# Optimization experiments

Hardware: AMD Instinct MI355X
Metric: run time of the kernel (lower is better)

Reference implementation:

```python
import jax, jax.numpy as jnp
import numpy as np

B, L, S, D, H, E, UV = 4, 2048, 2048, 1024, 8, 128, 128
ROT_DIM = H * E  # RotaryEmbedding(dim=qk_size*n_heads) applied on flattened dim


def gelu(x):
    return jax.nn.gelu(x, approximate=False)  # torch nn.GELU default (erf)


def rope(x):
    # x: [B, T, ROT_DIM]; interleaved-pair rotary (lucidrains rotary_embedding_torch default)
    T = x.shape[1]
    inv_freq = 1.0 / (10000.0 ** (jnp.arange(0, ROT_DIM, 2, dtype=jnp.float32) / ROT_DIM))
    freqs = jnp.arange(T, dtype=jnp.float32)[:, None] * inv_freq  # [T, ROT_DIM/2]
    cos = jnp.repeat(jnp.cos(freqs), 2, axis=-1)  # [T, ROT_DIM]
    sin = jnp.repeat(jnp.sin(freqs), 2, axis=-1)
    xp = x.reshape(*x.shape[:-1], ROT_DIM // 2, 2)
    x_rot = jnp.stack([-xp[..., 1], xp[..., 0]], axis=-1).reshape(x.shape)
    return x * cos + x_rot * sin


def setup_inputs() -> dict:
    key = jax.random.key(0)
    ks = jax.random.split(key, 16)
    n = lambda k, sh, s=1.0: jax.random.normal(k, sh, jnp.float32) * s
    w = 0.02
    return {
        "u": n(ks[0], (B, L, D)),
        "queries": n(ks[1], (B, L, D)),
        "keys": n(ks[2], (B, S, D)),
        "values": n(ks[3], (B, S, D)),
        "Wqk": n(ks[4], (D, H * E), w), "bqk": jnp.zeros((H * E,), jnp.float32),
        "Wv": n(ks[5], (D, H * UV), w), "bv": jnp.zeros((H * UV,), jnp.float32),
        "Wu": n(ks[6], (D, H * UV), w), "bu": jnp.zeros((H * UV,), jnp.float32),
        "Wo": n(ks[7], (H * UV, D), w), "bo": jnp.zeros((D,), jnp.float32),
        "q_gamma": jnp.ones((E,), jnp.float32), "q_beta": n(ks[8], (E,), w),
        "k_gamma": jnp.ones((E,), jnp.float32), "k_beta": n(ks[9], (E,), w),
    }


def _forward(u, queries, keys, values, Wqk, bqk, Wv, bv, Wu, bu, Wo, bo,
             q_gamma, q_beta, k_gamma, k_beta):
    # use_aff=True: shared qk projection + per-branch ScaleOffset over qk_size
    qk = gelu(queries @ Wqk + bqk)                      # [B,L,H*E]
    qk4 = qk.reshape(B, L, H, E)
    q = (qk4 * q_gamma + q_beta).reshape(B, L, H * E)
    k = (qk4 * k_gamma + k_beta).reshape(B, L, H * E)
    q = rope(q).reshape(B, L, H, E)
    k = rope(k).reshape(B, S, H, E)
    v = gelu(values @ Wv + bv).reshape(B, S, H, UV)
    # Conv1d(kernel_size=1) == pointwise linear over channels
    u_p = gelu(u @ Wu + bu).reshape(B, L, H, UV)
    scale = 1.0 / jnp.sqrt(jnp.float32(E))
    scores = jnp.einsum("blhe,bshe->bhls", q, k) * scale
    attn = jax.nn.softmax(scores, axis=-1)              # [B,H,L,S]
    ctx = jnp.einsum("bhls,bshd->blhd", attn, v)        # [B,L,H,UV]
    out = (u_p * ctx).reshape(B, L, H * UV)             # gate by u
    o = out @ Wo + bo                                   # [B,L,D]
    return o, attn


def reference(u, queries, keys, values, Wqk, bqk, Wv, bv, Wu, bu, Wo, bo,
              q_gamma, q_beta, k_gamma, k_beta):
    return _forward(u, queries, keys, values, Wqk, bqk, Wv, bv, Wu, bu, Wo, bo,
                    q_gamma, q_beta, k_gamma, k_beta)
```

## Files before the change

### kernel.cpp

```cpp
#include <hip/hip_runtime.h>
#include <hip/hip_bf16.h>
#include <math.h>

#define DEVI static __device__ __forceinline__

typedef __attribute__((ext_vector_type(4))) float f32x4;
typedef __attribute__((ext_vector_type(16))) float f32x16;
typedef __attribute__((ext_vector_type(8))) short bf16x8;
typedef __attribute__((ext_vector_type(4))) short bf16x4;

constexpr int Bc = 4, Lc = 2048, Sc = 2048, Dc = 1024, Hc = 8, Ec = 128, UVc = 128;
constexpr int HEc = Hc * Ec;
constexpr int BLc = Bc * Lc;

#define QSC (1.44269504088896340f / 11.31370849898476039f)

DEVI unsigned f2bf_bits(float f) {
  unsigned u = __builtin_bit_cast(unsigned, f);
  return (u + 0x7FFFu + ((u >> 16) & 1u)) >> 16;
}
DEVI short f2bf(float f) { return (short)f2bf_bits(f); }
DEVI float bf2f(short s) {
  return __builtin_bit_cast(float, (unsigned)((unsigned short)s) << 16);
}
DEVI float gelu_f(float x) { return 0.5f * x * (1.0f + erff(x * 0.7071067811865476f)); }

DEVI void gload16(const void* gsrc, void* ldst) {
  __builtin_amdgcn_global_load_lds(
      (const __attribute__((address_space(1))) unsigned*)gsrc,
      (__attribute__((address_space(3))) unsigned*)(ldst), 16, 0, 0);
}

DEVI f32x4 mfma16(bf16x8 a, bf16x8 b, f32x4 c) {
  return __builtin_amdgcn_mfma_f32_16x16x32_bf16(a, b, c, 0, 0, 0);
}
DEVI f32x16 mfma32(bf16x8 a, bf16x8 b, f32x16 c) {
  return __builtin_amdgcn_mfma_f32_32x32x16_bf16(a, b, c, 0, 0, 0);
}

__global__ void cvt3_kernel(const float* __restrict__ i0, const float* __restrict__ i1,
                            const float* __restrict__ i2, short* __restrict__ o0,
                            short* __restrict__ o1, short* __restrict__ o2) {
  const float* ins[3] = {i0, i1, i2};
  short* outs[3] = {o0, o1, o2};
  const float* in = ins[blockIdx.y];
  short* out = outs[blockIdx.y];
  size_t i = ((size_t)blockIdx.x * 256 + threadIdx.x) * 8;
  float4 f1 = *reinterpret_cast<const float4*>(in + i);
  float4 f2 = *reinterpret_cast<const float4*>(in + i + 4);
  uint4 pk;
  pk.x = f2bf_bits(f1.x) | (f2bf_bits(f1.y) << 16);
  pk.y = f2bf_bits(f1.z) | (f2bf_bits(f1.w) << 16);
  pk.z = f2bf_bits(f2.x) | (f2bf_bits(f2.y) << 16);
  pk.w = f2bf_bits(f2.z) | (f2bf_bits(f2.w) << 16);
  *reinterpret_cast<uint4*>(out + i) = pk;
}

__global__ void wt_trans_kernel(const float* __restrict__ W0, const float* __restrict__ W1,
                                const float* __restrict__ W2, const float* __restrict__ W3,
                                short* __restrict__ T0, short* __restrict__ T1,
                                short* __restrict__ T2, short* __restrict__ T3) {
  __shared__ float t[32][33];
  const float* Ws[4] = {W0, W1, W2, W3};
  short* Ts[4] = {T0, T1, T2, T3};
  const float* W = Ws[blockIdx.z];
  short* WT = Ts[blockIdx.z];
  int tx = threadIdx.x, ty = threadIdx.y;
  int n0 = blockIdx.x * 32, k0 = blockIdx.y * 32;
#pragma unroll
  for (int i = 0; i < 4; i++) {
    int r = ty + i * 8;
    t[r][tx] = W[(size_t)(k0 + r) * 1024 + n0 + tx];
  }
  __syncthreads();
#pragma unroll
  for (int i = 0; i < 4; i++) {
    int r = ty + i * 8;
    WT[(size_t)(n0 + r) * 1024 + k0 + tx] = f2bf(t[tx][r]);
  }
}

__global__ void rope_cs_kernel(float2* __restrict__ cs) {
  int idx = blockIdx.x * 256 + threadIdx.x;
  int t = idx >> 9, i = idx & 511;
  float inv = expf((float)i * (-9.210340371976184f / 512.0f));
  float sv, cv;
  sincosf((float)t * inv, &sv, &cv);
  cs[idx] = make_float2(cv, sv);
}

template <int EPI>
__global__ __launch_bounds__(256, 3) void gemm_kernel(
    const short* __restrict__ A, const short* __restrict__ BT,
    const float* __restrict__ bias, void* __restrict__ Cptr, int M, int N, int K) {
  __shared__ char smem[49152];
  const int tid = threadIdx.x;
  const int wave = tid >> 6, lane = tid & 63;
  const int lquad = lane >> 4, l15 = lane & 15;
  const int m0 = blockIdx.x * 128, n0 = blockIdx.y * 128;
  const int wr = wave >> 1, wc = wave & 1;
  f32x4 acc[4][4] = {};

  const int q0 = tid * 16, q1 = tid * 16 + 4096;
  const int r0 = q0 >> 6, o0 = (q0 & 63) ^ ((r0 & 3) << 4);
  const int r1 = q1 >> 6, o1 = (q1 & 63) ^ ((r1 & 3) << 4);
  const short* a0 = A + (size_t)(m0 + r0) * K + (o0 >> 1);
  const short* a1 = A + (size_t)(m0 + r1) * K + (o1 >> 1);
  const short* b0 = BT + (size_t)(n0 + r0) * K + (o0 >> 1);
  const short* b1 = BT + (size_t)(n0 + r1) * K + (o1 >> 1);

#define G_STAGE(buf, kt)                     \
  {                                          \
    char* As_ = smem + (buf)*8192;           \
    char* Bs_ = smem + 24576 + (buf)*8192;   \
    gload16(a0 + (kt), As_ + q0);            \
    gload16(a1 + (kt), As_ + q1);            \
    gload16(b0 + (kt), Bs_ + q0);            \
    gload16(b1 + (kt), Bs_ + q1);            \
  }

  G_STAGE(0, 0);
  G_STAGE(1, 32);
  asm volatile("s_waitcnt vmcnt(4)" ::: "memory");
  __builtin_amdgcn_s_barrier();

  const int NT = K >> 5;
  int cur = 0;
  for (int t = 0; t < NT; t++) {
    int nb = cur + 2;
    if (nb >= 3) nb -= 3;
    G_STAGE(nb, (t + 2 < NT) ? (t + 2) * 32 : 0);
    __builtin_amdgcn_sched_barrier(0);
    const char* As_ = smem + cur * 8192;
    const char* Bs_ = smem + 24576 + cur * 8192;
    const int ko = lquad * 16;
    bf16x8 a[4], b[4];
#pragma unroll
    for (int f = 0; f < 4; f++) {
      int ra = wr * 64 + f * 16 + l15;
      a[f] = *reinterpret_cast<const bf16x8*>(As_ + ra * 64 + (ko ^ ((ra & 3) << 4)));
      int rb = wc * 64 + f * 16 + l15;
      b[f] = *reinterpret_cast<const bf16x8*>(Bs_ + rb * 64 + (ko ^ ((rb & 3) << 4)));
    }
#pragma unroll
    for (int mf = 0; mf < 4; mf++)
#pragma unroll
      for (int nf = 0; nf < 4; nf++)
        acc[mf][nf] = mfma16(a[mf], b[nf], acc[mf][nf]);
    asm volatile("s_waitcnt vmcnt(4) lgkmcnt(0)" ::: "memory");
    __builtin_amdgcn_sched_barrier(0);
    __builtin_amdgcn_s_barrier();
    cur = (cur == 2) ? 0 : cur + 1;
  }
#undef G_STAGE

#pragma unroll
  for (int mf = 0; mf < 4; mf++) {
#pragma unroll
    for (int nf = 0; nf < 4; nf++) {
      const int mrow = m0 + wr * 64 + mf * 16 + 4 * lquad;
      const int ncol = n0 + wc * 64 + nf * 16 + l15;
      const float bval = bias[ncol];
      if constexpr (EPI == 3) {
        int hh = ncol >> 7, dd = ncol & 127;
        int bb = mrow >> 11, ss = mrow & 2047;
        bf16x4 gv;
#pragma unroll
        for (int r = 0; r < 4; r++) gv[r] = f2bf(gelu_f(acc[mf][nf][r] + bval));
        *reinterpret_cast<bf16x4*>((short*)Cptr + (((size_t)bb * 8 + hh) * 128 + dd) * 2048 + ss) = gv;
      } else if constexpr (EPI == 1) {
#pragma unroll
        for (int r = 0; r < 4; r++)
          ((short*)Cptr)[(size_t)(mrow + r) * N + ncol] = f2bf(gelu_f(acc[mf][nf][r] + bval));
      } else {
#pragma unroll
        for (int r = 0; r < 4; r++)
          ((float*)Cptr)[(size_t)(mrow + r) * N + ncol] = acc[mf][nf][r] + bval;
      }
    }
  }
}

__global__ void rope_apply_kernel(const short* __restrict__ qkg,
                                  const float2* __restrict__ cstab,
                                  const float* __restrict__ qg, const float* __restrict__ qb,
                                  const float* __restrict__ kg, const float* __restrict__ kb,
                                  short* __restrict__ qo, short* __restrict__ ko) {
  int tid = blockIdx.x * 256 + threadIdx.x;
  size_t base = (size_t)tid * 8;
  int bl = (int)(base >> 10);
  int rem = (int)(base & 1023);
  int e0 = rem & 127;
  int t = bl & 2047;
  int pf = rem >> 1;
  uint4 raw = *reinterpret_cast<const uint4*>(qkg + base);
  short sh[8];
  *reinterpret_cast<uint4*>(sh) = raw;
  const float* csf = (const float*)cstab + (size_t)t * 1024 + 2 * pf;
  float4 p01 = *reinterpret_cast<const float4*>(csf);
  float4 p23 = *reinterpret_cast<const float4*>(csf + 4);
  float C[4] = {p01.x, p01.z, p23.x, p23.z};
  float Sn[4] = {p01.y, p01.w, p23.y, p23.w};
  float4 qga = *reinterpret_cast<const float4*>(qg + e0);
  float4 qgb = *reinterpret_cast<const float4*>(qg + e0 + 4);
  float4 qba = *reinterpret_cast<const float4*>(qb + e0);
  float4 qbb = *reinterpret_cast<const float4*>(qb + e0 + 4);
  float4 kga = *reinterpret_cast<const float4*>(kg + e0);
  float4 kgb = *reinterpret_cast<const float4*>(kg + e0 + 4);
  float4 kba = *reinterpret_cast<const float4*>(kb + e0);
  float4 kbb = *reinterpret_cast<const float4*>(kb + e0 + 4);
  float QG[8] = {qga.x, qga.y, qga.z, qga.w, qgb.x, qgb.y, qgb.z, qgb.w};
  float QB[8] = {qba.x, qba.y, qba.z, qba.w, qbb.x, qbb.y, qbb.z, qbb.w};
  float KG[8] = {kga.x, kga.y, kga.z, kga.w, kgb.x, kgb.y, kgb.z, kgb.w};
  float KB[8] = {kba.x, kba.y, kba.z, kba.w, kbb.x, kbb.y, kbb.z, kbb.w};
  short qsh[8], ksh[8];
#pragma unroll
  for (int j = 0; j < 4; j++) {
    float x0 = bf2f(sh[2 * j]), x1 = bf2f(sh[2 * j + 1]);
    float q0 = x0 * QG[2 * j] + QB[2 * j];
    float q1 = x1 * QG[2 * j + 1] + QB[2 * j + 1];
    qsh[2 * j] = f2bf((q0 * C[j] - q1 * Sn[j]) * QSC);
    qsh[2 * j + 1] = f2bf((q1 * C[j] + q0 * Sn[j]) * QSC);
    float k0v = x0 * KG[2 * j] + KB[2 * j];
    float k1v = x1 * KG[2 * j + 1] + KB[2 * j + 1];
    ksh[2 * j] = f2bf(k0v * C[j] - k1v * Sn[j]);
    ksh[2 * j + 1] = f2bf(k1v * C[j] + k0v * Sn[j]);
  }
  *reinterpret_cast<uint4*>(qo + base) = *reinterpret_cast<uint4*>(qsh);
  *reinterpret_cast<uint4*>(ko + base) = *reinterpret_cast<uint4*>(ksh);
}

__global__ __launch_bounds__(256, 3) void passa_kernel(
    const short* __restrict__ qs, const short* __restrict__ ks,
    float* __restrict__ rcpbuf) {
  __shared__ char smem[49152];
  const int bid = blockIdx.x;
  const int xcd = bid & 7, jj = bid >> 3;
  const int bh = xcd * 4 + (jj >> 4);
  const int lblk = jj & 15;
  const int b = bh >> 3, h = bh & 7;
  const int l0 = lblk * 128;
  const int tid = threadIdx.x;
  const int wave = tid >> 6, lane = tid & 63;
  const int l31 = lane & 31, lhg = lane >> 5;

  const short* ksrc[4];
  int kq[4];
#pragma unroll
  for (int i = 0; i < 4; i++) {
    int q = i * 4096 + tid * 16;
    kq[i] = q;
    int row = q >> 8, off = (q & 255) ^ ((row & 7) << 4);
    ksrc[i] = ks + (((size_t)b * Sc + row) * Hc + h) * Ec + (off >> 1);
  }

  bf16x8 qf[8];
  {
    const char* qp = (const char*)(qs + (((size_t)b * Lc + l0 + wave * 32 + l31) * Hc + h) * Ec);
#pragma unroll
    for (int kt = 0; kt < 8; kt++)
      qf[kt] = *reinterpret_cast<const bf16x8*>(qp + kt * 32 + 16 * lhg);
  }
  __builtin_amdgcn_sched_barrier(0);

#define STAGE_A(buf, s0)                                  \
  {                                                       \
    char* Kb_ = smem + (buf)*16384;                       \
    gload16(ksrc[0] + (size_t)(s0)*1024, Kb_ + kq[0]);    \
    gload16(ksrc[1] + (size_t)(s0)*1024, Kb_ + kq[1]);    \
    gload16(ksrc[2] + (size_t)(s0)*1024, Kb_ + kq[2]);    \
    gload16(ksrc[3] + (size_t)(s0)*1024, Kb_ + kq[3]);    \
  }

  STAGE_A(0, 0);
  STAGE_A(1, 64);
  asm volatile("s_waitcnt vmcnt(4)" ::: "memory");
  __builtin_amdgcn_s_barrier();
  float ra = 0.f, rb = 0.f, rc = 0.f, rd = 0.f;
  int cur = 0;
  for (int t = 0; t < 32; t++) {
    int nb = cur + 2;
    if (nb >= 3) nb -= 3;
    STAGE_A(nb, (t + 2 < 32) ? (t + 2) * 64 : 0);
    __builtin_amdgcn_sched_barrier(0);
    const char* KB_ = smem + cur * 16384;
    f32x16 d0 = {}, d1 = {};
    __builtin_amdgcn_s_setprio(1);
#pragma unroll
    for (int kt = 0; kt < 8; kt++) {
      int row0 = l31, row1 = 32 + l31;
      bf16x8 k0 = *reinterpret_cast<const bf16x8*>(
          KB_ + row0 * 256 + ((kt * 32 + 16 * lhg) ^ ((row0 & 7) << 4)));
      bf16x8 k1 = *reinterpret_cast<const bf16x8*>(
          KB_ + row1 * 256 + ((kt * 32 + 16 * lhg) ^ ((row1 & 7) << 4)));
      d0 = mfma32(k0, qf[kt], d0);
      d1 = mfma32(k1, qf[kt], d1);
    }
    __builtin_amdgcn_s_setprio(0);
#pragma unroll
    for (int r = 0; r < 16; r += 4) {
      ra += exp2f(d0[r]) + exp2f(d1[r]);
      rb += exp2f(d0[r + 1]) + exp2f(d1[r + 1]);
      rc += exp2f(d0[r + 2]) + exp2f(d1[r + 2]);
      rd += exp2f(d0[r + 3]) + exp2f(d1[r + 3]);
    }
    asm volatile("s_waitcnt vmcnt(4) lgkmcnt(0)" ::: "memory");
    __builtin_amdgcn_sched_barrier(0);
    __builtin_amdgcn_s_barrier();
    cur = (cur == 2) ? 0 : cur + 1;
  }
#undef STAGE_A
  float rs = (ra + rb) + (rc + rd);
  rs += __shfl_xor(rs, 32);
  if (lane < 32)
    rcpbuf[(size_t)bh * Lc + l0 + wave * 32 + l31] = 1.0f / rs;
}

__global__ __launch_bounds__(256, 3) void attn_kernel(
    const short* __restrict__ qs, const short* __restrict__ ks,
    const short* __restrict__ vT, const short* __restrict__ up,
    const float* __restrict__ rcpbuf, float* __restrict__ attn_out,
    short* __restrict__ gate) {
  __shared__ char smem[49152];
  const int bid = blockIdx.x;
  const int xcd = bid & 7, jj = bid >> 3;
  const int bh = xcd * 4 + (jj >> 4);
  const int lblk = jj & 15;
  const int b = bh >> 3, h = bh & 7;
  const int l0 = lblk * 128;
  const int tid = threadIdx.x;
  const int wave = tid >> 6, lane = tid & 63;
  const int lquad = lane >> 4, l15 = lane & 15;

  const short* ksrc[2];
  int kq[2];
#pragma unroll
  for (int i = 0; i < 2; i++) {
    int q = i * 4096 + tid * 16;
    kq[i] = q;
    int row = q >> 8, off = (q & 255) ^ ((row & 7) << 4);
    ksrc[i] = ks + (((size_t)b * Sc + row) * Hc + h) * Ec + (off >> 1);
  }
  const short* vsrc[2];
  int vq[2];
#pragma unroll
  for (int i = 0; i < 2; i++) {
    int q = i * 4096 + tid * 16;
    vq[i] = q;
    int rv = q >> 6;
    int j = (q >> 4) & 3;
    int c = (j - (rv & 3)) & 3;
    vsrc[i] = vT + ((size_t)bh * UVc + rv) * Sc + (c << 3);
  }

  bf16x8 qf[2][4];
  float rcp[2];
#pragma unroll
  for (int cf = 0; cf < 2; cf++) {
    int lrow = l0 + wave * 32 + cf * 16 + l15;
    const short* qp = qs + (((size_t)b * Lc + lrow) * Hc + h) * Ec;
#pragma unroll
    for (int kt = 0; kt < 4; kt++)
      qf[cf][kt] = *reinterpret_cast<const bf16x8*>(qp + kt * 32 + lquad * 8);
    rcp[cf] = rcpbuf[(size_t)bh * Lc + lrow];
  }
  __builtin_amdgcn_sched_barrier(0);

#define STAGE_B(buf, s0)                                  \
  {                                                       \
    char* Kb_ = smem + (buf)*8192;                        \
    char* Vb_ = smem + 24576 + (buf)*8192;                \
    gload16(ksrc[0] + (size_t)(s0)*1024, Kb_ + kq[0]);    \
    gload16(ksrc[1] + (size_t)(s0)*1024, Kb_ + kq[1]);    \
    gload16(vsrc[0] + (s0), Vb_ + vq[0]);                 \
    gload16(vsrc[1] + (s0), Vb_ + vq[1]);                 \
  }

  STAGE_B(0, 0);
  STAGE_B(1, 32);
  asm volatile("s_waitcnt vmcnt(4)" ::: "memory");
  __builtin_amdgcn_s_barrier();
  f32x4 ctx[8][2] = {};
  int cur = 0;
  for (int t = 0; t < 64; t++) {
    const int s0 = t * 32;
    int nb = cur + 2;
    if (nb >= 3) nb -= 3;
    STAGE_B(nb, (t + 2 < 64) ? s0 + 64 : 0);
    __builtin_amdgcn_sched_barrier(0);
    const char* KB_ = smem + cur * 8192;
    const char* VB_ = smem + 24576 + cur * 8192;
    f32x4 d[2][2] = {};
    __builtin_amdgcn_s_setprio(1);
#pragma unroll
    for (int kt = 0; kt < 4; kt++)
#pragma unroll
      for (int sf = 0; sf < 2; sf++) {
        int row = sf * 16 + l15;
        bf16x8 kf = *reinterpret_cast<const bf16x8*>(
            KB_ + row * 256 + ((kt * 64 + lquad * 16) ^ ((row & 7) << 4)));
        d[sf][0] = mfma16(kf, qf[0][kt], d[sf][0]);
        d[sf][1] = mfma16(kf, qf[1][kt], d[sf][1]);
      }
    __builtin_amdgcn_s_setprio(0);
#pragma unroll
    for (int sf = 0; sf < 2; sf++)
#pragma unroll
      for (int cf = 0; cf < 2; cf++)
#pragma unroll
        for (int r = 0; r < 4; r++)
          d[sf][cf][r] = exp2f(d[sf][cf][r]) * rcp[cf];
    bf16x8 pb[2];
#pragma unroll
    for (int cf = 0; cf < 2; cf++)
#pragma unroll
      for (int r = 0; r < 4; r++) {
        pb[cf][r] = f2bf(d[0][cf][r]);
        pb[cf][4 + r] = f2bf(d[1][cf][r]);
      }
    __builtin_amdgcn_s_setprio(1);
#pragma unroll
    for (int df = 0; df < 8; df++) {
      int dd = df * 16 + l15;
      const char* vrow = VB_ + dd * 64;
      int half = (lquad & 1) * 8;
      int clo = ((lquad >> 1) + (dd & 3)) & 3;
      int chi = ((lquad >> 1) + 2 + (dd & 3)) & 3;
      bf16x4 lo = *reinterpret_cast<const bf16x4*>(vrow + clo * 16 + half);
      bf16x4 hi = *reinterpret_cast<const bf16x4*>(vrow + chi * 16 + half);
      bf16x8 vf = __builtin_shufflevector(lo, hi, 0, 1, 2, 3, 4, 5, 6, 7);
      ctx[df][0] = mfma16(vf, pb[0], ctx[df][0]);
      ctx[df][1] = mfma16(vf, pb[1], ctx[df][1]);
    }
    __builtin_amdgcn_s_setprio(0);
#pragma unroll
    for (int cf = 0; cf < 2; cf++) {
      int lrow = l0 + wave * 32 + cf * 16 + l15;
      float* arow = attn_out + ((size_t)bh * Lc + lrow) * Sc + s0 + lquad * 4;
      __builtin_nontemporal_store(d[0][cf], reinterpret_cast<f32x4*>(arow));
      __builtin_nontemporal_store(d[1][cf], reinterpret_cast<f32x4*>(arow + 16));
    }
    asm volatile("s_waitcnt vmcnt(8) lgkmcnt(0)" ::: "memory");
    __builtin_amdgcn_sched_barrier(0);
    __builtin_amdgcn_s_barrier();
    cur = (cur == 2) ? 0 : cur + 1;
  }
#undef STAGE_B

#pragma unroll
  for (int cf = 0; cf < 2; cf++) {
    int lrow = l0 + wave * 32 + cf * 16 + l15;
    size_t base = ((size_t)b * Lc + lrow) * HEc + h * UVc;
    const short* ub = up + base;
    short* gp = gate + base;
#pragma unroll
    for (int df = 0; df < 8; df++) {
      int doff = df * 16 + lquad * 4;
      bf16x4 uv = *reinterpret_cast<const bf16x4*>(ub + doff);
      bf16x4 gv;
#pragma unroll
      for (int r = 0; r < 4; r++)
        gv[r] = f2bf(bf2f(uv[r]) * ctx[df][cf][r]);
      *reinterpret_cast<bf16x4*>(gp + doff) = gv;
    }
  }
}

extern "C" void kernel_launch(void* const* d_in, const int* in_sizes, int n_in,
                              void* d_out, int out_size, void* d_ws, size_t ws_size,
                              hipStream_t stream) {
  const float* u_in = (const float*)d_in[0];
  const float* qry = (const float*)d_in[1];
  const float* vals = (const float*)d_in[3];
  const float* Wqk = (const float*)d_in[4];
  const float* bqk = (const float*)d_in[5];
  const float* Wv = (const float*)d_in[6];
  const float* bv = (const float*)d_in[7];
  const float* Wu = (const float*)d_in[8];
  const float* bu = (const float*)d_in[9];
  const float* Wo = (const float*)d_in[10];
  const float* bo = (const float*)d_in[11];
  const float* qg = (const float*)d_in[12];
  const float* qb = (const float*)d_in[13];
  const float* kg = (const float*)d_in[14];
  const float* kb = (const float*)d_in[15];

  char* w = (char*)d_ws;
  short* WT0 = (short*)w; w += (size_t)1024 * 1024 * 2;
  short* WT1 = (short*)w; w += (size_t)1024 * 1024 * 2;
  short* WT2 = (short*)w; w += (size_t)1024 * 1024 * 2;
  short* WT3 = (short*)w; w += (size_t)1024 * 1024 * 2;
  float2* cstab = (float2*)w; w += (size_t)2048 * 512 * 8;
  float* rcpb = (float*)w; w += (size_t)32 * 2048 * 4;
  const size_t BUF = (size_t)BLc * HEc * 2;
  short* C1 = (short*)w; w += BUF;
  short* C2 = (short*)w; w += BUF;
  short* C3 = (short*)w; w += BUF;
  short* qkg = (short*)w; w += BUF;
  short* qbf = (short*)w; w += BUF;
  short* vTb = (short*)w; w += BUF;
  short* upb = (short*)w; w += BUF;
  short* kbf = qkg;
  short* gtb = C1;

  float* o_out = (float*)d_out;
  float* attn_out = o_out + (size_t)BLc * Dc;

  dim3 tb(32, 8);
  cvt3_kernel<<<dim3(4096, 3), 256, 0, stream>>>(qry, vals, u_in, C1, C2, C3);
  wt_trans_kernel<<<dim3(32, 32, 4), tb, 0, stream>>>(Wqk, Wv, Wu, Wo, WT0, WT1, WT2, WT3);
  rope_cs_kernel<<<4096, 256, 0, stream>>>(cstab);

  gemm_kernel<1><<<dim3(64, 8), 256, 0, stream>>>(C1, WT0, bqk, qkg, BLc, HEc, Dc);
  rope_apply_kernel<<<4096, 256, 0, stream>>>(qkg, cstab, qg, qb, kg, kb, qbf, kbf);
  passa_kernel<<<512, 256, 0, stream>>>(qbf, kbf, rcpb);
  gemm_kernel<3><<<dim3(64, 8), 256, 0, stream>>>(C2, WT1, bv, vTb, BLc, HEc, Dc);
  gemm_kernel<1><<<dim3(64, 8), 256, 0, stream>>>(C3, WT2, bu, upb, BLc, HEc, Dc);
  attn_kernel<<<512, 256, 0, stream>>>(qbf, kbf, vTb, upb, rcpb, attn_out, gtb);
  gemm_kernel<0><<<dim3(64, 8), 256, 0, stream>>>(gtb, WT3, bo, o_out, BLc, Dc, HEc);
}
```

Baseline: 411.2 us.

## Reorder attention loop stores and prefetch, fuse prep kernels, approximate GELU erf

In the attention loop, the attn probability stores are now issued right after the exp step, and the K/V prefetch for the next stage moves to the end of the iteration instead of the start. The aim is to change how global stores and loads overlap with the MFMA work. The weight transpose and RoPE cos/sin table kernels are merged into one launch to save a kernel launch. GELU now uses an Abramowitz–Stegun polynomial erf with a hardware reciprocal and exp2 in place of erff, which is cheaper but adds a small approximation error.

```diff
diff --git a/kernel.cpp b/kernel.cpp
--- a/kernel.cpp
+++ b/kernel.cpp
@@ -23,7 +23,17 @@
 DEVI float bf2f(short s) {
   return __builtin_bit_cast(float, (unsigned)((unsigned short)s) << 16);
 }
-DEVI float gelu_f(float x) { return 0.5f * x * (1.0f + erff(x * 0.7071067811865476f)); }
+DEVI float gelu_f(float x) {
+  float z = fabsf(x) * 0.7071067811865476f;
+  float t = __builtin_amdgcn_rcpf(1.0f + 0.3275911f * z);
+  float p = t * (0.254829592f +
+            t * (-0.284496736f +
+            t * (1.421413741f +
+            t * (-1.453152027f + t * 1.061405429f))));
+  float e = exp2f(-z * z * 1.4426950408889634f);
+  float er = copysignf(1.0f - p * e, x);
+  return 0.5f * x * (1.0f + er);
+}
 
 DEVI void gload16(const void* gsrc, void* ldst) {
   __builtin_amdgcn_global_load_lds(
@@ -56,37 +66,42 @@
   *reinterpret_cast<uint4*>(out + i) = pk;
 }
 
-__global__ void wt_trans_kernel(const float* __restrict__ W0, const float* __restrict__ W1,
-                                const float* __restrict__ W2, const float* __restrict__ W3,
-                                short* __restrict__ T0, short* __restrict__ T1,
-                                short* __restrict__ T2, short* __restrict__ T3) {
-  __shared__ float t[32][33];
+__global__ void prep_kernel(const float* __restrict__ W0, const float* __restrict__ W1,
+                            const float* __restrict__ W2, const float* __restrict__ W3,
+                            short* __restrict__ T0, short* __restrict__ T1,
+                            short* __restrict__ T2, short* __restrict__ T3,
+                            float2* __restrict__ cs) {
+  int tx = threadIdx.x, ty = threadIdx.y;
+  if (blockIdx.z == 4) {
+    int base = (blockIdx.y * 32 + blockIdx.x) * 256 + ty * 32 + tx;
+#pragma unroll
+    for (int j = 0; j < 4; j++) {
+      int idx = base + j * 262144;
+      int t = idx >> 9, i = idx & 511;
+      float inv = expf((float)i * (-9.210340371976184f / 512.0f));
+      float sv, cv;
+      sincosf((float)t * inv, &sv, &cv);
+      cs[idx] = make_float2(cv, sv);
+    }
+    return;
+  }
+  __shared__ float tbuf[32][33];
   const float* Ws[4] = {W0, W1, W2, W3};
   short* Ts[4] = {T0, T1, T2, T3};
   const float* W = Ws[blockIdx.z];
   short* WT = Ts[blockIdx.z];
-  int tx = threadIdx.x, ty = threadIdx.y;
   int n0 = blockIdx.x * 32, k0 = blockIdx.y * 32;
 #pragma unroll
   for (int i = 0; i < 4; i++) {
     int r = ty + i * 8;
-    t[r][tx] = W[(size_t)(k0 + r) * 1024 + n0 + tx];
+    tbuf[r][tx] = W[(size_t)(k0 + r) * 1024 + n0 + tx];
   }
   __syncthreads();
 #pragma unroll
   for (int i = 0; i < 4; i++) {
     int r = ty + i * 8;
-    WT[(size_t)(n0 + r) * 1024 + k0 + tx] = f2bf(t[tx][r]);
-  }
-}
-
-__global__ void rope_cs_kernel(float2* __restrict__ cs) {
-  int idx = blockIdx.x * 256 + threadIdx.x;
-  int t = idx >> 9, i = idx & 511;
-  float inv = expf((float)i * (-9.210340371976184f / 512.0f));
-  float sv, cv;
-  sincosf((float)t * inv, &sv, &cv);
-  cs[idx] = make_float2(cv, sv);
+    WT[(size_t)(n0 + r) * 1024 + k0 + tx] = f2bf(tbuf[tx][r]);
+  }
 }
 
 template <int EPI>
@@ -384,10 +399,6 @@
   int cur = 0;
   for (int t = 0; t < 64; t++) {
     const int s0 = t * 32;
-    int nb = cur + 2;
-    if (nb >= 3) nb -= 3;
-    STAGE_B(nb, (t + 2 < 64) ? s0 + 64 : 0);
-    __builtin_amdgcn_sched_barrier(0);
     const char* KB_ = smem + cur * 8192;
     const char* VB_ = smem + 24576 + cur * 8192;
     f32x4 d[2][2] = {};
@@ -410,6 +421,13 @@
 #pragma unroll
         for (int r = 0; r < 4; r++)
           d[sf][cf][r] = exp2f(d[sf][cf][r]) * rcp[cf];
+#pragma unroll
+    for (int cf = 0; cf < 2; cf++) {
+      int lrow = l0 + wave * 32 + cf * 16 + l15;
+      float* arow = attn_out + ((size_t)bh * Lc + lrow) * Sc + s0 + lquad * 4;
+      __builtin_nontemporal_store(d[0][cf], reinterpret_cast<f32x4*>(arow));
+      __builtin_nontemporal_store(d[1][cf], reinterpret_cast<f32x4*>(arow + 16));
+    }
     bf16x8 pb[2];
 #pragma unroll
     for (int cf = 0; cf < 2; cf++)
@@ -433,12 +451,10 @@
       ctx[df][1] = mfma16(vf, pb[1], ctx[df][1]);
     }
     __builtin_amdgcn_s_setprio(0);
-#pragma unroll
-    for (int cf = 0; cf < 2; cf++) {
-      int lrow = l0 + wave * 32 + cf * 16 + l15;
-      float* arow = attn_out + ((size_t)bh * Lc + lrow) * Sc + s0 + lquad * 4;
-      __builtin_nontemporal_store(d[0][cf], reinterpret_cast<f32x4*>(arow));
-      __builtin_nontemporal_store(d[1][cf], reinterpret_cast<f32x4*>(arow + 16));
+    {
+      int nb = cur + 2;
+      if (nb >= 3) nb -= 3;
+      STAGE_B(nb, (t + 2 < 64) ? s0 + 64 : 0);
     }
     asm volatile("s_waitcnt vmcnt(8) lgkmcnt(0)" ::: "memory");
     __builtin_amdgcn_sched_barrier(0);
@@ -508,8 +524,7 @@
 
   dim3 tb(32, 8);
   cvt3_kernel<<<dim3(4096, 3), 256, 0, stream>>>(qry, vals, u_in, C1, C2, C3);
-  wt_trans_kernel<<<dim3(32, 32, 4), tb, 0, stream>>>(Wqk, Wv, Wu, Wo, WT0, WT1, WT2, WT3);
-  rope_cs_kernel<<<4096, 256, 0, stream>>>(cstab);
+  prep_kernel<<<dim3(32, 32, 5), tb, 0, stream>>>(Wqk, Wv, Wu, Wo, WT0, WT1, WT2, WT3, cstab);
 
   gemm_kernel<1><<<dim3(64, 8), 256, 0, stream>>>(C1, WT0, bqk, qkg, BLc, HEc, Dc);
   rope_apply_kernel<<<4096, 256, 0, stream>>>(qkg, cstab, qg, qb, kg, kb, qbf, kbf);
```

After: 387.2 us. 1.06x faster.
